# Kernel tuning notes

Measured on AMD Instinct MI355X. Metric: run time of the kernel, lower is better.

## Reference

```python
import jax, jax.numpy as jnp
import numpy as np

N_NODES, N_EDGES = 10000, 100000
NODE_DIM, NUM_BASIS = 128, 20
MULS = {0: 128, 1: 64, 2: 32}            # 128x0e + 64x1e + 32x2e
NUM_IRREPS = 224                          # total multiplicity count
HIDDEN = NODE_DIM + NUM_IRREPS            # 352
SPH_DIM = 128 * 1 + 64 * 3 + 32 * 5       # 480
LN_EPS = 1e-5

def _s2_basis():
    # orthonormal (Frobenius) basis of symmetric traceless 3x3 matrices (real l=2)
    s = np.zeros((5, 3, 3)); r2 = 1.0 / np.sqrt(2.0)
    s[0, 0, 1] = s[0, 1, 0] = r2
    s[1, 1, 2] = s[1, 2, 1] = r2
    s[2] = np.diag([-1.0, -1.0, 2.0]) / np.sqrt(6.0)
    s[3, 0, 2] = s[3, 2, 0] = r2
    s[4] = np.diag([1.0, -1.0, 0.0]) * r2
    return s

def _cg_tables():
    # real Clebsch-Gordan tensors for l<=2 built from the invariant tensors
    # delta, Levi-Civita, and the symmetric-traceless basis; unit Frobenius norm (e3nn w3j convention)
    e3 = np.zeros((3, 3, 3))
    e3[0, 1, 2] = e3[1, 2, 0] = e3[2, 0, 1] = 1.0
    e3[0, 2, 1] = e3[2, 1, 0] = e3[1, 0, 2] = -1.0
    S = _s2_basis(); I3 = np.eye(3); I5 = np.eye(5)
    nrm = lambda c: (c / np.linalg.norm(c)).astype(np.float32)
    cg = {(0, 0, 0): np.ones((1, 1, 1), np.float32)}
    cg[(0, 1, 1)] = nrm(I3[None]); cg[(1, 0, 1)] = nrm(I3[:, None, :]); cg[(1, 1, 0)] = nrm(I3[:, :, None])
    cg[(0, 2, 2)] = nrm(I5[None]); cg[(2, 0, 2)] = nrm(I5[:, None, :]); cg[(2, 2, 0)] = nrm(I5[:, :, None])
    cg[(1, 1, 1)] = nrm(e3)
    cg[(1, 1, 2)] = nrm(np.transpose(S, (1, 2, 0)))
    cg[(1, 2, 1)] = nrm(np.transpose(S, (1, 0, 2)))
    cg[(2, 1, 1)] = nrm(S)
    cg[(2, 2, 1)] = nrm(np.einsum('ijk,Mil,Nlj->MNk', e3, S, S))
    cg[(1, 2, 2)] = nrm(np.einsum('iab,Mac,Ncb->iMN', e3, S, S))
    cg[(2, 1, 2)] = nrm(np.einsum('jab,Mac,Ncb->MjN', e3, S, S))
    cg[(2, 2, 2)] = nrm(np.einsum('Mab,Nbc,Pca->MNP', S, S, S))
    return cg

CG = _cg_tables()
PATHS = [(0, 0, 0), (1, 1, 0), (2, 2, 0),
         (0, 1, 1), (1, 0, 1), (1, 1, 1), (1, 2, 1), (2, 1, 1), (2, 2, 1),
         (0, 2, 2), (1, 1, 2), (1, 2, 2), (2, 0, 2), (2, 1, 2), (2, 2, 2)]
FAN = {0: 224, 1: 384, 2: 352}   # e3nn 'element' path-norm fan-in per output irrep
TP_NUMW = sum(MULS[l1] * MULS[l3] for (l1, _, l3) in PATHS)

def _layernorm(x, w, b):
    mu = x.mean(-1, keepdims=True)
    var = ((x - mu) ** 2).mean(-1, keepdims=True)
    return (x - mu) * jax.lax.rsqrt(var + LN_EPS) * w + b

def _o3_layernorm(x, w, b):
    # equivariant layer norm: per-irrep RMS over (mul, m); mean-centering + bias only for scalars
    n = x.shape[0]; outs = []; off = 0; woff = 0
    for l in (0, 1, 2):
        mul, d = MULS[l], 2 * l + 1
        f = x[:, off:off + mul * d].reshape(n, mul, d)
        if l == 0:
            f = f - f.mean(axis=1, keepdims=True)
        nrm = (f * f).mean(axis=(1, 2), keepdims=True)
        f = f * jax.lax.rsqrt(nrm + LN_EPS) * w[woff:woff + mul][None, :, None]
        if l == 0:
            f = f + b[None, :, None]
        outs.append(f.reshape(n, mul * d)); off += mul * d; woff += mul
    return jnp.concatenate(outs, -1)

def _fc_tp(x1, x2, tp_w):
    # FullyConnectedTensorProduct(128x0e+64x1e+32x2e, 1x0e+1x1e+1x2e -> 128x0e+64x1e+32x2e)
    outs = {0: 0.0, 1: 0.0, 2: 0.0}; off = 0
    for (l1, l2, l3) in PATHS:
        m1, m3 = MULS[l1], MULS[l3]
        W = tp_w[off:off + m1 * m3].reshape(m1, m3); off += m1 * m3
        pw = float(np.sqrt((2 * l3 + 1) / FAN[l3]))
        outs[l3] = outs[l3] + pw * jnp.einsum('eum,en,mnk,uw->ewk', x1[l1], x2[l2], jnp.asarray(CG[(l1, l2, l3)]), W, optimize=True)
    e = x2[0].shape[0]
    return jnp.concatenate([outs[l].reshape(e, -1) for l in (0, 1, 2)], -1)

def _forward(x_scalar, x_spherical, rbf, rsh, ln_w, ln_b, o3_w, o3_b,
             mlp_w1, mlp_b1, mlp_w2, mlp_b2, rbf_w, tp_w, edge_index):
    scalar_in = _layernorm(x_scalar, ln_w, ln_b)                # [N,128]
    spherical_in = _o3_layernorm(x_spherical, o3_w, o3_b)       # [N,480]
    h = jax.nn.silu(scalar_in @ mlp_w1 + mlp_b1)
    scalar_out = h @ mlp_w2 + mlp_b2                            # [N,352]
    filt = rbf @ rbf_w                                          # [E,352]
    dst, src = edge_index[0], edge_index[1]
    fo = scalar_out[src] * filt                                 # gather + RBF filter
    gate, msg_scalar = fo[:, :NUM_IRREPS], fo[:, NUM_IRREPS:]
    sph = spherical_in[src]                                     # [E,480]
    e = sph.shape[0]
    # ElementwiseTensorProduct(edge_irreps, 224x0e): per-channel scalar gating
    x1 = {0: (sph[:, :128] * gate[:, :128])[:, :, None],
          1: sph[:, 128:320].reshape(e, 64, 3) * gate[:, 128:192, None],
          2: sph[:, 320:480].reshape(e, 32, 5) * gate[:, 192:224, None]}
    x2 = {0: rsh[:, :1], 1: rsh[:, 1:4], 2: rsh[:, 4:9]}
    msg_sph = _fc_tp(x1, x2, tp_w)                              # [E,480]
    new_scalar = scalar_in.at[dst].add(msg_scalar)
    new_spherical = spherical_in.at[dst].add(msg_sph)
    return new_scalar, new_spherical

def setup_inputs():
    key = jax.random.key(0)
    ks = jax.random.split(key, 9)
    return {
        'x_scalar': jax.random.normal(ks[0], (N_NODES, NODE_DIM), jnp.float32),
        'x_spherical': jax.random.normal(ks[1], (N_NODES, SPH_DIM), jnp.float32),
        'rbf': jax.random.uniform(ks[2], (N_EDGES, NUM_BASIS), jnp.float32),
        'rsh': jax.random.normal(ks[3], (N_EDGES, 9), jnp.float32),
        'edge_index': jax.random.randint(ks[4], (2, N_EDGES), 0, N_NODES, dtype=jnp.int32),
        'ln_w': jnp.ones((NODE_DIM,), jnp.float32),
        'ln_b': jnp.zeros((NODE_DIM,), jnp.float32),
        'o3_w': jnp.ones((NUM_IRREPS,), jnp.float32),
        'o3_b': jnp.zeros((128,), jnp.float32),
        'mlp_w1': jax.random.normal(ks[5], (NODE_DIM, NODE_DIM), jnp.float32) / np.sqrt(NODE_DIM),
        'mlp_b1': jnp.zeros((NODE_DIM,), jnp.float32),
        'mlp_w2': jax.random.normal(ks[6], (NODE_DIM, HIDDEN), jnp.float32) / np.sqrt(NODE_DIM),
        'mlp_b2': jnp.zeros((HIDDEN,), jnp.float32),
        'rbf_w': jax.random.normal(ks[7], (NUM_BASIS, HIDDEN), jnp.float32) / np.sqrt(NUM_BASIS),
        'tp_w': jax.random.normal(ks[8], (TP_NUMW,), jnp.float32),
    }

def reference(x_scalar, x_spherical, rbf, rsh, edge_index, ln_w, ln_b, o3_w, o3_b,
              mlp_w1, mlp_b1, mlp_w2, mlp_b2, rbf_w, tp_w):
    return _forward(x_scalar, x_spherical, rbf, rsh, ln_w, ln_b, o3_w, o3_b,
                    mlp_w1, mlp_b1, mlp_w2, mlp_b2, rbf_w, tp_w, edge_index)
```

## Files before the change

### kernel.cpp

```cpp
#include <hip/hip_runtime.h>

#define NN 10000
#define NE 100000
#define ND 128
#define NB 20
#define NIR 224
#define NH 352
#define SD 480
#define BS 512
#define ET 16
#define NTILES (NE / ET)

#define CR   0.70710678118654752f
#define CA   0.40824829046386302f
#define HA   0.20412414523193151f
#define HR   0.35355339059327376f
#define C110 0.57735026918962576f
#define C220 0.44721359549995794f
#define C111 0.40824829046386302f
#define C11X 0.44721359549995794f
#define C221 0.36514837167011074f
#define C222 0.58554004376912270f
#define S32  0.86602540378443865f
#define PW0  0.066815310478106094f
#define PW1  0.088388347648318447f
#define PW2  0.11918321088232916f

typedef __bf16 v8bf __attribute__((ext_vector_type(8)));
typedef unsigned short us8v __attribute__((ext_vector_type(8)));
typedef float f32x4 __attribute__((ext_vector_type(4)));

__device__ __forceinline__ unsigned short f2bfc(float f) {
  __bf16 h = (__bf16)f;
  return __builtin_bit_cast(unsigned short, h);
}
__device__ __forceinline__ float bf2f(unsigned short h) {
  unsigned int u = ((unsigned int)h) << 16;
  return __builtin_bit_cast(float, u);
}

__device__ __forceinline__ float warpReduceSum(float v) {
  #pragma unroll
  for (int off = 32; off > 0; off >>= 1) v += __shfl_down(v, off, 64);
  return v;
}

__device__ __forceinline__ int t2tT(int t) {
  if (t < 128) return t;
  if (t < 320) { int c = t - 128; return 128 + (c % 3) * 64 + c / 3; }
  int c = t - 320; return 320 + (c % 5) * 32 + c / 5;
}

__global__ __launch_bounds__(256) void sort_hist(const int* __restrict__ ei, int* __restrict__ cnt) {
  int e = blockIdx.x * 256 + threadIdx.x;
  if (e < NE) atomicAdd(&cnt[ei[e]], 1);
}

__global__ __launch_bounds__(1024) void sort_scan(const int* __restrict__ cnt, int* __restrict__ cursor) {
  __shared__ int part[1024];
  const int t = threadIdx.x;
  int loc[10]; int s = 0;
  #pragma unroll
  for (int j = 0; j < 10; ++j) { int idx = t * 10 + j; int v = (idx < NN) ? cnt[idx] : 0; loc[j] = s; s += v; }
  part[t] = s; __syncthreads();
  for (int d = 1; d < 1024; d <<= 1) {
    int v = (t >= d) ? part[t - d] : 0; __syncthreads();
    part[t] += v; __syncthreads();
  }
  int off = part[t] - s;
  #pragma unroll
  for (int j = 0; j < 10; ++j) { int idx = t * 10 + j; if (idx < NN) cursor[idx] = off + loc[j]; }
}

__global__ __launch_bounds__(256) void sort_scatter(
    const int* __restrict__ ei, int* __restrict__ cursor, int* __restrict__ es_eid) {
  int e = blockIdx.x * 256 + threadIdx.x;
  if (e < NE) {
    int d = ei[e];
    int pos = atomicAdd(&cursor[d], 1);
    es_eid[pos] = e;
  }
}

__global__ __launch_bounds__(128) void node_ln_kernel(
    const float* __restrict__ xs, const float* __restrict__ xsph,
    const float* __restrict__ lnw, const float* __restrict__ lnb,
    const float* __restrict__ o3w, const float* __restrict__ o3b,
    float* __restrict__ s_in, float* __restrict__ sphT,
    float* __restrict__ out0)
{
  const int n = blockIdx.x, t = threadIdx.x;
  __shared__ float red[4];

  auto reduce2 = [&](float a, float b) {
// ... 43 lines not shown
    const float* __restrict__ b2, float* __restrict__ s_out)
{
  __shared__ float sIn[NPB][ND];
  __shared__ float sH[NPB][ND];
  const int t = threadIdx.x;
  const int n0 = blockIdx.x * NPB;
  for (int i = t; i < NPB * ND; i += 256) sIn[i >> 7][i & 127] = s_in[n0 * ND + i];
  __syncthreads();
  {
    const int j = t & 127, g = t >> 7;
    float acc[4] = {0.f, 0.f, 0.f, 0.f};
    for (int k = 0; k < ND; ++k) {
      float w = w1[k * ND + j];
      #pragma unroll
      for (int i = 0; i < 4; ++i) acc[i] = fmaf(sIn[g + 2 * i][k], w, acc[i]);
    }
    #pragma unroll
    for (int i = 0; i < 4; ++i) {
      float z = acc[i] + b1[j];
      sH[g + 2 * i][j] = z / (1.f + __expf(-z));
    }
  }
  __syncthreads();
  for (int jb = 0; jb < 2; ++jb) {
    int j = jb * 256 + t;
    if (j < NH) {
      float acc[NPB];
      #pragma unroll
      for (int i = 0; i < NPB; ++i) acc[i] = b2[j];
      for (int k = 0; k < ND; ++k) {
        float w = w2[k * NH + j];
        #pragma unroll
        for (int i = 0; i < NPB; ++i) acc[i] = fmaf(sH[i][k], w, acc[i]);
      }
      #pragma unroll
      for (int i = 0; i < NPB; ++i) s_out[(n0 + i) * NH + j] = acc[i];
    }
  }
}

__device__ __forceinline__ float wc0(const float* w, int u, int j) {
  int off = (u < 128) ? u * 128 : (u < 192) ? 16384 + (u - 128) * 128 : 24576 + (u - 192) * 128;
  return w[off + j];
}
__device__ __forceinline__ float wc1(const float* w, int u, int j) {
  int off = (u < 128) ? 28672 + u * 64 : (u < 192) ? 36864 + (u - 128) * 64
          : (u < 256) ? 40960 + (u - 192) * 64 : (u < 320) ? 45056 + (u - 256) * 64
          : (u < 352) ? 49152 + (u - 320) * 64 : 51200 + (u - 352) * 64;
  return w[off + j];
}
__device__ __forceinline__ float wc2(const float* w, int u, int j) {
  int off = (u < 128) ? 53248 + u * 32 : (u < 192) ? 57344 + (u - 128) * 32
          : (u < 256) ? 59392 + (u - 192) * 32 : (u < 288) ? 61440 + (u - 256) * 32
          : (u < 320) ? 62464 + (u - 288) * 32 : 63488 + (u - 320) * 32;
  return w[off + j];
}

__global__ __launch_bounds__(256) void prep_w_kernel(
    const float* __restrict__ tpw, const float* __restrict__ rbf_w,
    unsigned short* __restrict__ W0g, unsigned short* __restrict__ W1g,
    unsigned short* __restrict__ W2g, unsigned short* __restrict__ Wfq)
{
  int gid = blockIdx.x * 256 + threadIdx.x;
  int i = gid & 7, lane = (gid >> 3) & 63;
  int r = lane & 15, kl = lane >> 4;
  if (gid < 28672) {
    int fid = gid >> 9, kk = fid >> 3, wid = fid & 7;
    W0g[gid] = f2bfc(wc0(tpw, kk * 32 + kl * 8 + i, wid * 16 + r));
  } else if (gid < 53248) {
    int g = gid - 28672, fid = g >> 9, kk = fid >> 2, nt = fid & 3;
    W1g[g] = f2bfc(wc1(tpw, kk * 32 + kl * 8 + i, nt * 16 + r));
  } else if (gid < 65536) {
    int g = gid - 53248, fid = g >> 9, q = fid >> 2, kh = (fid >> 1) & 1, ntc = fid & 1;
    int kk = kh * 6 + q;
    W2g[g] = (kk < 11) ? f2bfc(wc2(tpw, kk * 32 + kl * 8 + i, ntc * 16 + r)) : (unsigned short)0;
  } else if (gid < 77824) {
    int g = gid - 65536, fid = g >> 9, q = fid >> 3, wid = fid & 7;
    int t22 = wid + q * 8, k = kl * 8 + i;
    Wfq[g] = (t22 < 22 && k < 20) ? f2bfc(rbf_w[k * NH + t22 * 16 + r]) : (unsigned short)0;
  }
}

template<int M>
__device__ __forceinline__ void emit_dot(unsigned short* dst, const unsigned short* x1,
                                         const int* offs, const float* cf) {
  us8v xv[M];
  #pragma unroll
  for (int m = 0; m < M; ++m) xv[m] = *(const us8v*)&x1[offs[m]];
  v8bf o;
  #pragma unroll
  for (int i = 0; i < 8; ++i) {
    float a = 0.f;
    #pragma unroll
    for (int m = 0; m < M; ++m) a = fmaf(cf[m], bf2f(xv[m][i]), a);
    o[i] = (__bf16)a;
  }
  *(us8v*)dst = __builtin_bit_cast(us8v, o);
}

#define TSW(e, idx) ((idx) ^ (((e) & 7) << 3))

__device__ __forceinline__ void build0_item(unsigned short* Tb, const unsigned short* x1,
                                            const float* R, int e, int ub) {
  int u0 = ub * 8;
  unsigned short* dst = Tb + TSW(e, e * 384 + u0);
  if (u0 < 128) {
    float cf[1] = { PW0 * R[0] };
    int offs[1] = { u0 };
    emit_dot<1>(dst, x1, offs, cf);
  } else if (u0 < 192) {
    int m0 = u0 - 128;
    float cf[3] = { PW0 * C110 * R[1], PW0 * C110 * R[2], PW0 * C110 * R[3] };
    int offs[3] = { 128 + m0, 192 + m0, 256 + m0 };
    emit_dot<3>(dst, x1, offs, cf);
  } else {
    int m0 = u0 - 192;
    float cf[5] = { PW0 * C220 * R[4], PW0 * C220 * R[5], PW0 * C220 * R[6],
                    PW0 * C220 * R[7], PW0 * C220 * R[8] };
    int offs[5] = { 320 + m0, 352 + m0, 384 + m0, 416 + m0, 448 + m0 };
    emit_dot<5>(dst, x1, offs, cf);
  }
}

template<int k>
__device__ __forceinline__ void build1_item(unsigned short* Tb, const unsigned short* x1,
                                            const float* R, int e, int ub) {
  int u0 = ub * 8;
  unsigned short* dst = Tb + TSW(e, e * 384 + u0);
  const float s = R[0], v0 = R[1], v1 = R[2], v2 = R[3];
  const float w0 = R[4], w1 = R[5], w2 = R[6], w3 = R[7], w4 = R[8];
  if (u0 < 128) {
    float cf[1] = { PW1 * C110 * R[1 + k] };
    int offs[1] = { u0 };
    emit_dot<1>(dst, x1, offs, cf);
  } else if (u0 < 192) {
    float cf[1] = { PW1 * C110 * s };
    int offs[1] = { 128 + k * 64 + (u0 - 128) };
    emit_dot<1>(dst, x1, offs, cf);
  } else if (u0 < 256) {
    constexpr int ka = (k + 1) % 3, kb = (k + 2) % 3;
    int m0 = u0 - 192;
    float cf[2] = { PW1 * C111 * R[1 + kb], -PW1 * C111 * R[1 + ka] };
    int offs[2] = { 128 + ka * 64 + m0, 128 + kb * 64 + m0 };
    emit_dot<2>(dst, x1, offs, cf);
  } else if (u0 < 320) {
    int m0 = u0 - 256;
    float cf[3];
    if constexpr (k == 0) { cf[0] = PW1*C11X*(-CA*w2 + CR*w4); cf[1] = PW1*C11X*CR*w0; cf[2] = PW1*C11X*CR*w3; }
    else if constexpr (k == 1) { cf[0] = PW1*C11X*CR*w0; cf[1] = PW1*C11X*(-CA*w2 - CR*w4); cf[2] = PW1*C11X*CR*w1; }
    else { cf[0] = PW1*C11X*CR*w3; cf[1] = PW1*C11X*CR*w1; cf[2] = PW1*C11X*2.f*CA*w2; }
    int offs[3] = { 128 + m0, 192 + m0, 256 + m0 };
    emit_dot<3>(dst, x1, offs, cf);
  } else if (u0 < 352) {
    int m0 = u0 - 320;
    if constexpr (k == 0) {
      float cf[4] = { PW1*C11X*CR*v1, PW1*C11X*(-CA*v0), PW1*C11X*CR*v2, PW1*C11X*CR*v0 };
      int offs[4] = { 320 + m0, 384 + m0, 416 + m0, 448 + m0 };
      emit_dot<4>(dst, x1, offs, cf);
    } else if constexpr (k == 1) {
      float cf[4] = { PW1*C11X*CR*v0, PW1*C11X*CR*v2, PW1*C11X*(-CA*v1), PW1*C11X*(-CR*v1) };
      int offs[4] = { 320 + m0, 352 + m0, 384 + m0, 448 + m0 };
      emit_dot<4>(dst, x1, offs, cf);
    } else {
      float cf[3] = { PW1*C11X*CR*v1, PW1*C11X*2.f*CA*v2, PW1*C11X*CR*v0 };
      int offs[3] = { 352 + m0, 384 + m0, 416 + m0 };
      emit_dot<3>(dst, x1, offs, cf);
    }
  } else {
    int m0 = u0 - 352;
    if constexpr (k == 0) {
      float cf[5] = { PW1*C221*0.5f*w3, PW1*C221*(S32*w2 + 0.5f*w4), PW1*C221*(-S32*w1),
                      PW1*C221*(-0.5f*w0), PW1*C221*(-0.5f*w1) };
      int offs[5] = { 320 + m0, 352 + m0, 384 + m0, 416 + m0, 448 + m0 };
      emit_dot<5>(dst, x1, offs, cf);
    } else if constexpr (k == 1) {
      float cf[5] = { PW1*C221*(-0.5f*w1), PW1*C221*0.5f*w0, PW1*C221*S32*w3,
                      PW1*C221*(-S32*w2 + 0.5f*w4), PW1*C221*(-0.5f*w3) };
      int offs[5] = { 320 + m0, 352 + m0, 384 + m0, 416 + m0, 448 + m0 };
      emit_dot<5>(dst, x1, offs, cf);
    } else {
      float cf[4] = { PW1*C221*(-w4), PW1*C221*(-0.5f*w3), PW1*C221*0.5f*w1, PW1*C221*w0 };
      int offs[4] = { 320 + m0, 352 + m0, 416 + m0, 448 + m0 };
      emit_dot<4>(dst, x1, offs, cf);
    }
  }
}

template<int K>
__device__ __forceinline__ void build2_item(unsigned short* Tb, const unsigned short* x1,
                                            const float* R, int e, int ub) {
  int u0 = ub * 8;
  unsigned short* dst = Tb + TSW(e, e * 384 + u0);
  const float s = R[0], v0 = R[1], v1 = R[2], v2 = R[3];
  const float w0 = R[4], w1 = R[5], w2 = R[6], w3 = R[7], w4 = R[8];
  if (u0 < 128) {
    float cf[1] = { PW2 * C220 * R[4 + K] };
    int offs[1] = { u0 };
    emit_dot<1>(dst, x1, offs, cf);
  } else if (u0 < 192) {
    int m0 = u0 - 128;
    if constexpr (K == 0) {
      float cf[2] = { PW2*C11X*CR*v1, PW2*C11X*CR*v0 };
      int offs[2] = { 128 + m0, 192 + m0 };
      emit_dot<2>(dst, x1, offs, cf);
    } else if constexpr (K == 1) {
      float cf[2] = { PW2*C11X*CR*v2, PW2*C11X*CR*v1 };
      int offs[2] = { 192 + m0, 256 + m0 };
      emit_dot<2>(dst, x1, offs, cf);
    } else if constexpr (K == 2) {
      float cf[3] = { PW2*C11X*(-CA*v0), PW2*C11X*(-CA*v1), PW2*C11X*2.f*CA*v2 };
      int offs[3] = { 128 + m0, 192 + m0, 256 + m0 };
      emit_dot<3>(dst, x1, offs, cf);
    } else if constexpr (K == 3) {
      float cf[2] = { PW2*C11X*CR*v2, PW2*C11X*CR*v0 };
      int offs[2] = { 128 + m0, 256 + m0 };
      emit_dot<2>(dst, x1, offs, cf);
    } else {
      float cf[2] = { PW2*C11X*CR*v0, PW2*C11X*(-CR*v1) };
      int offs[2] = { 128 + m0, 192 + m0 };
      emit_dot<2>(dst, x1, offs, cf);
    }
  } else if (u0 < 256) {
    int m0 = u0 - 192;
    if constexpr (K == 2) {
      float cf[2] = { PW2*C221*S32*w1, PW2*C221*(-S32*w3) };
      int offs[2] = { 128 + m0, 192 + m0 };
      emit_dot<2>(dst, x1, offs, cf);
    } else {
      float cf[3];
      if constexpr (K == 0) { cf[0]=PW2*C221*(-0.5f*w3); cf[1]=PW2*C221*0.5f*w1; cf[2]=PW2*C221*w4; }
      else if constexpr (K == 1) { cf[0]=PW2*C221*(-S32*w2 - 0.5f*w4); cf[1]=PW2*C221*(-0.5f*w0); cf[2]=PW2*C221*0.5f*w3; }
      else if constexpr (K == 3) { cf[0]=PW2*C221*0.5f*w0; cf[1]=PW2*C221*(S32*w2 - 0.5f*w4); cf[2]=PW2*C221*(-0.5f*w1); }
      else { cf[0]=PW2*C221*0.5f*w1; cf[1]=PW2*C221*0.5f*w3; cf[2]=PW2*C221*(-w0); }
      int offs[3] = { 128 + m0, 192 + m0, 256 + m0 };
      emit_dot<3>(dst, x1, offs, cf);
    }
  } else if (u0 < 288) {
    int m0 = u0 - 256;
    float cf[1] = { PW2 * C220 * s };
    int offs[1] = { 320 + K * 32 + m0 };
    emit_dot<1>(dst, x1, offs, cf);
  } else if (u0 < 320) {
    int m0 = u0 - 288;
    if constexpr (K == 0) {
      float cf[3] = { PW2*C221*0.5f*v1, PW2*C221*(-0.5f*v0), PW2*C221*v2 };
      int offs[3] = { 352 + m0, 416 + m0, 448 + m0 };
      emit_dot<3>(dst, x1, offs, cf);
    } else if constexpr (K == 1) {
      float cf[4] = { PW2*C221*(-0.5f*v1), PW2*C221*(-S32*v0), PW2*C221*0.5f*v2, PW2*C221*(-0.5f*v0) };
      int offs[4] = { 320 + m0, 384 + m0, 416 + m0, 448 + m0 };
      emit_dot<4>(dst, x1, offs, cf);
    } else if constexpr (K == 2) {
      float cf[2] = { PW2*C221*S32*v0, PW2*C221*(-S32*v1) };
      int offs[2] = { 352 + m0, 416 + m0 };
      emit_dot<2>(dst, x1, offs, cf);
    } else if constexpr (K == 3) {
      float cf[4] = { PW2*C221*0.5f*v0, PW2*C221*(-0.5f*v2), PW2*C221*S32*v1, PW2*C221*(-0.5f*v1) };
      int offs[4] = { 320 + m0, 352 + m0, 384 + m0, 448 + m0 };
      emit_dot<4>(dst, x1, offs, cf);
    } else {
      float cf[3] = { PW2*C221*(-v2), PW2*C221*0.5f*v0, PW2*C221*0.5f*v1 };
      int offs[3] = { 320 + m0, 352 + m0, 416 + m0 };
      emit_dot<3>(dst, x1, offs, cf);
    }
  } else {
    int m0 = u0 - 320;
    if constexpr (K == 0) {
      float cf[4] = { PW2*C222*(-CA*w2), PW2*C222*HR*w3, PW2*C222*(-CA*w0), PW2*C222*HR*w1 };
      int offs[4] = { 320 + m0, 352 + m0, 384 + m0, 416 + m0 };
      emit_dot<4>(dst, x1, offs, cf);
    } else if constexpr (K == 4) {
      float cf[4] = { PW2*C222*(-HR*w1), PW2*C222*(-CA*w4), PW2*C222*HR*w3, PW2*C222*(-CA*w2) };
      int offs[4] = { 352 + m0, 384 + m0, 416 + m0, 448 + m0 };
      emit_dot<4>(dst, x1, offs, cf);
    } else {
      float cf[5];
      if constexpr (K == 1) { cf[0]=PW2*C222*HR*w3; cf[1]=PW2*C222*(HA*w2 - HR*w4); cf[2]=PW2*C222*HA*w1; cf[3]=PW2*C222*HR*w0; cf[4]=PW2*C222*(-HR*w1); }
      else if constexpr (K == 2) { cf[0]=PW2*C222*(-CA*w0); cf[1]=PW2*C222*HA*w1; cf[2]=PW2*C222*CA*w2; cf[3]=PW2*C222*HA*w3; cf[4]=PW2*C222*(-CA*w4); }
      else { cf[0]=PW2*C222*HR*w1; cf[1]=PW2*C222*HR*w0; cf[2]=PW2*C222*HA*w3; cf[3]=PW2*C222*(HA*w2 + HR*w4); cf[4]=PW2*C222*HR*w3; }
      int offs[5] = { 320 + m0, 352 + m0, 384 + m0, 416 + m0, 448 + m0 };
      emit_dot<5>(dst, x1, offs, cf);
    }
  }
}

__global__ __launch_bounds__(BS, 4) void tp_fused_kernel(
    const float* __restrict__ rbf, const float* __restrict__ rsh,
    const int* __restrict__ ei, const float* __restrict__ s_out,
    const float* __restrict__ sphT,
    const unsigned short* __restrict__ W0g, const unsigned short* __restrict__ W1g,
    const unsigned short* __restrict__ W2g, const unsigned short* __restrict__ Wfq,
    float* __restrict__ out0, unsigned short* __restrict__ msgT)
{
  __shared__ __align__(16) unsigned char smem[65216];
  unsigned short* S0 = (unsigned short*)smem;
  unsigned short* S1 = (unsigned short*)(smem + 12288);
  unsigned short* S2 = (unsigned short*)(smem + 24576);
  unsigned short* S3 = (unsigned short*)(smem + 36864);
  unsigned short* gateU = (unsigned short*)smem;
  unsigned short* rbfpadU = (unsigned short*)(smem + 12288);
  unsigned short* X1u = (unsigned short*)(smem + 49152);
  float* RshF = (float*)(smem + 64512);
  int* EdstS = (int*)(smem + 65088);
  int* EsrcS = (int*)(smem + 65152);

  const int tid = threadIdx.x;
  const int wid = tid >> 6, lane = tid & 63;
  const int r = lane & 15, kl = lane >> 4;
  const int be = tid >> 5, th = tid & 31;

  auto MFMA = [](v8bf a, v8bf b, f32x4 c) {
    return __builtin_amdgcn_mfma_f32_16x16x32_bf16(a, b, c, 0, 0, 0);
  };
  auto ldw = [&](const unsigned short* base, int fid) {
    return __builtin_bit_cast(v8bf, *(const us8v*)&base[fid * 512 + lane * 8]);
  };

  auto mfma_l0 = [&](const unsigned short* T, long ebase) {
    f32x4 acc = {0.f, 0.f, 0.f, 0.f};
    #pragma unroll
    for (int kk = 0; kk < 7; ++kk) {
      v8bf b = ldw(W0g, kk * 8 + wid);
      us8v a = *(const us8v*)&T[TSW(r, r * 384 + kl * 8 + kk * 32)];
      acc = MFMA(__builtin_bit_cast(v8bf, a), b, acc);
    }
    int col = wid * 16 + r;
    #pragma unroll
    for (int j = 0; j < 4; ++j)
      msgT[(ebase + kl * 4 + j) * SD + col] = f2bfc(acc[j]);
  };

  auto mfma_l1w = [&](const unsigned short* T, int k, int nt, long ebase) {
    f32x4 acc = {0.f, 0.f, 0.f, 0.f};
    #pragma unroll
    for (int kk = 0; kk < 12; ++kk) {
      v8bf b = ldw(W1g, kk * 4 + nt);
      us8v a = *(const us8v*)&T[TSW(r, r * 384 + kl * 8 + kk * 32)];
      acc = MFMA(__builtin_bit_cast(v8bf, a), b, acc);
    }
    int col = 128 + k * 64 + nt * 16 + r;
    #pragma unroll
    for (int j = 0; j < 4; ++j)
      msgT[(ebase + kl * 4 + j) * SD + col] = f2bfc(acc[j]);
  };

  auto mfma_l2w = [&](const unsigned short* T, int K, int ntc, long ebase) {
    f32x4 acc = {0.f, 0.f, 0.f, 0.f};
    #pragma unroll
    for (int kk = 0; kk < 11; ++kk) {
      v8bf b = ldw(W2g, (kk % 6) * 4 + (kk / 6) * 2 + ntc);
      us8v a = *(const us8v*)&T[TSW(r, r * 384 + kk * 32 + kl * 8)];
      acc = MFMA(__builtin_bit_cast(v8bf, a), b, acc);
    }
    int col = 320 + K * 32 + ntc * 16 + r;
    #pragma unroll
    for (int j = 0; j < 4; ++j)
      msgT[(ebase + kl * 4 + j) * SD + col] = f2bfc(acc[j]);
  };

  for (int tile = blockIdx.x; tile < NTILES; tile += gridDim.x) {
    const int e0 = tile * ET;
    const long ebase = e0;
    for (int i = tid; i < ET; i += BS) { EdstS[i] = ei[e0 + i]; EsrcS[i] = ei[NE + e0 + i]; }
    for (int i = tid; i < ET * 9; i += BS) RshF[i] = rsh[(long)e0 * 9 + i];
    for (int i = tid; i < ET * 32; i += BS) {
      int e = i >> 5, b = i & 31;
      rbfpadU[e * 40 + b] = (b < 20) ? f2bfc(rbf[(long)(e0 + e) * NB + b]) : (unsigned short)0;
    }
    __syncthreads();
    {
      us8v ra = *(const us8v*)&rbfpadU[r * 40 + kl * 8];
      v8bf av = __builtin_bit_cast(v8bf, ra);
      #pragma unroll
      for (int q = 0; q < 3; ++q) {
        int t22 = wid + q * 8;
        if (t22 < 22) {
          v8bf b = ldw(Wfq, q * 8 + wid);
          f32x4 acc = {0.f, 0.f, 0.f, 0.f};
          acc = MFMA(av, b, acc);
          int gi = t22 * 16 + r;
          #pragma unroll
          for (int j = 0; j < 4; ++j) {
            int e = kl * 4 + j;
            float so = s_out[(long)EsrcS[e] * NH + gi];
            float val = acc[j] * so;
            if (t22 < 14) gateU[e * 232 + gi] = f2bfc(val);
            else unsafeAtomicAdd(&out0[(long)EdstS[e] * ND + (gi - 224)], val);
          }
        }
      }
    }
    __syncthreads();
    float Rr[9];
    #pragma unroll
    for (int j = 0; j < 9; ++j) Rr[j] = RshF[be * 9 + j];
    const unsigned short* x1p = &X1u[be * 480];
    {
      long srow = (long)EsrcS[be] * SD;
      #pragma unroll
      for (int rep = 0; rep < 2; ++rep) {
        int cb = th + rep * 32;
        if (rep == 0 || th < 28) {
          int c0 = cb * 8;
          int gidx = (c0 < 128) ? c0 : (c0 < 320) ? 128 + (c0 & 63) : 192 + (c0 & 31);
          us8v gv = *(const us8v*)&gateU[be * 232 + gidx];
          const float4 sa = *(const float4*)&sphT[srow + c0];
          const float4 sb = *(const float4*)&sphT[srow + c0 + 4];
          float sv[8] = {sa.x, sa.y, sa.z, sa.w, sb.x, sb.y, sb.z, sb.w};
          v8bf o;
          #pragma unroll
          for (int i = 0; i < 8; ++i) o[i] = (__bf16)(sv[i] * bf2f(gv[i]));
          *(us8v*)&X1u[be * 480 + c0] = __builtin_bit_cast(us8v, o);
        }
      }
    }
    __syncthreads();
    if (th < 28) build0_item(S0, x1p, Rr, be, th);
    __syncthreads();
    build1_item<0>(S1, x1p, Rr, be, th);
    if (th < 16) build1_item<0>(S1, x1p, Rr, be, th + 32);
    else         build1_item<1>(S2, x1p, Rr, be, th - 16);
    build1_item<1>(S2, x1p, Rr, be, th + 16);
    mfma_l0(S0, ebase);
    __syncthreads();
    build1_item<2>(S3, x1p, Rr, be, th);
    if (th < 16) build1_item<2>(S3, x1p, Rr, be, th + 32);
    else         build2_item<0>(S0, x1p, Rr, be, th - 16);
    if (th < 28) build2_item<0>(S0, x1p, Rr, be, th + 16);
    if (wid < 4) mfma_l1w(S1, 0, wid, ebase);
    else         mfma_l1w(S2, 1, wid - 4, ebase);
    __syncthreads();
    build2_item<1>(S1, x1p, Rr, be, th);
    if (th < 12) build2_item<1>(S1, x1p, Rr, be, th + 32);
    else         build2_item<2>(S2, x1p, Rr, be, th - 12);
    if (th < 24) build2_item<2>(S2, x1p, Rr, be, th + 20);
    if (wid < 4)      mfma_l1w(S3, 2, wid, ebase);
    else if (wid < 6) mfma_l2w(S0, 0, wid - 4, ebase);
    __syncthreads();
    build2_item<3>(S3, x1p, Rr, be, th);
    if (th < 12) build2_item<3>(S3, x1p, Rr, be, th + 32);
    else         build2_item<4>(S0, x1p, Rr, be, th - 12);
    if (th < 24) build2_item<4>(S0, x1p, Rr, be, th + 20);
    if (wid < 2)      mfma_l2w(S1, 1, wid, ebase);
    else if (wid < 4) mfma_l2w(S2, 2, wid - 2, ebase);
    __syncthreads();
    if (wid < 2)      mfma_l2w(S3, 3, wid, ebase);
    else if (wid < 4) mfma_l2w(S0, 4, wid - 2, ebase);
    __syncthreads();
  }
}

__global__ __launch_bounds__(512) void gather_kernel(
    const float* __restrict__ sphT, const unsigned short* __restrict__ msgT,
    const int* __restrict__ cnt, const int* __restrict__ cursor,
    const int* __restrict__ es_eid, float* __restrict__ out1)
{
  __shared__ float sumT[SD];
  __shared__ int eids[160];
  __shared__ int s_deg;
  const int n = blockIdx.x, t = threadIdx.x;
  if (t == 0) {
    int d = cnt[n];
    s_deg = (d > 160) ? 160 : d;
  }
  __syncthreads();
  int deg = s_deg;
  int start = cursor[n] - cnt[n];
  for (int i = t; i < deg; i += 512) eids[i] = es_eid[start + i];
  __syncthreads();
  if (t < 240) {
    float a0 = 0.f, a1 = 0.f;
    for (int i = 0; i < deg; ++i) {
      unsigned v = *(const unsigned*)&msgT[(long)eids[i] * SD + 2 * t];
      a0 += bf2f((unsigned short)(v & 0xffffu));
      a1 += bf2f((unsigned short)(v >> 16));
    }
    sumT[2 * t] = a0; sumT[2 * t + 1] = a1;
  }
  __syncthreads();
  if (t < SD) {
    int tT = t2tT(t);
    out1[(long)n * SD + t] = sphT[(long)n * SD + tT] + sumT[tT];
  }
}

extern "C" void kernel_launch(void* const* d_in, const int* in_sizes, int n_in,
                              void* d_out, int out_size, void* d_ws, size_t ws_size,
                              hipStream_t stream)
{
  const float* xs   = (const float*)d_in[0];
  const float* xsph = (const float*)d_in[1];
  const float* rbf  = (const float*)d_in[2];
  const float* rsh  = (const float*)d_in[3];
  const int*   ei   = (const int*)d_in[4];
  const float* lnw  = (const float*)d_in[5];
  const float* lnb  = (const float*)d_in[6];
  const float* o3w  = (const float*)d_in[7];
  const float* o3b  = (const float*)d_in[8];
  const float* w1   = (const float*)d_in[9];
  const float* b1   = (const float*)d_in[10];
  const float* w2   = (const float*)d_in[11];
  const float* b2   = (const float*)d_in[12];
  const float* rbfw = (const float*)d_in[13];
  const float* tpw  = (const float*)d_in[14];

  float* out0 = (float*)d_out;
  float* out1 = out0 + (size_t)NN * ND;

  float* ws      = (float*)d_ws;
  float* s_in    = ws;
  float* sphT    = ws + (size_t)NN * ND;
  float* s_out   = ws + (size_t)NN * (ND + SD);
  unsigned short* msgT = (unsigned short*)(ws + (size_t)NN * (ND + SD + NH));
  unsigned short* wbase = msgT + (size_t)NE * SD;
  unsigned short* W0g = wbase;
  unsigned short* W1g = wbase + 28672;
  unsigned short* W2g = wbase + 53248;
  unsigned short* Wfq = wbase + 65536;
  int* ibase  = (int*)(wbase + 77824);
  int* cnt    = ibase;
  int* cursor = ibase + 10000;
  int* es_eid = ibase + 20000;

  hipMemsetAsync(cnt, 0, (size_t)NN * sizeof(int), stream);
  sort_hist<<<(NE + 255) / 256, 256, 0, stream>>>(ei, cnt);
  sort_scan<<<1, 1024, 0, stream>>>(cnt, cursor);
  sort_scatter<<<(NE + 255) / 256, 256, 0, stream>>>(ei, cursor, es_eid);
  prep_w_kernel<<<304, 256, 0, stream>>>(tpw, rbfw, W0g, W1g, W2g, Wfq);
  node_ln_kernel<<<NN, 128, 0, stream>>>(xs, xsph, lnw, lnb, o3w, o3b, s_in, sphT, out0);
  mlp_kernel<<<NN / NPB, 256, 0, stream>>>(s_in, w1, b1, w2, b2, s_out);
  tp_fused_kernel<<<512, BS, 0, stream>>>(rbf, rsh, ei, s_out, sphT,
                                          W0g, W1g, W2g, Wfq, out0, msgT);
  gather_kernel<<<NN, 512, 0, stream>>>(sphT, msgT, cnt, cursor, es_eid, out1);
}
```

Measured before the change: 660.6 us.

## Build MFMA A-fragments in registers instead of staging through LDS

```diff
diff --git a/kernel.cpp b/kernel.cpp
--- a/kernel.cpp
+++ b/kernel.cpp
@@ -10,6 +10,7 @@
 #define BS 512
 #define ET 16
 #define NTILES (NE / ET)
+#define XSTR 488
 
 #define CR   0.70710678118654752f
 #define CA   0.40824829046386302f
@@ -219,8 +220,7 @@
 }
 
 template<int M>
-__device__ __forceinline__ void emit_dot(unsigned short* dst, const unsigned short* x1,
-                                         const int* offs, const float* cf) {
+__device__ __forceinline__ v8bf dot_frag(const unsigned short* x1, const int* offs, const float* cf) {
   us8v xv[M];
   #pragma unroll
   for (int m = 0; m < M; ++m) xv[m] = *(const us8v*)&x1[offs[m]];
@@ -232,137 +232,127 @@
     for (int m = 0; m < M; ++m) a = fmaf(cf[m], bf2f(xv[m][i]), a);
     o[i] = (__bf16)a;
   }
-  *(us8v*)dst = __builtin_bit_cast(us8v, o);
-}
-
-#define TSW(e, idx) ((idx) ^ (((e) & 7) << 3))
-
-__device__ __forceinline__ void build0_item(unsigned short* Tb, const unsigned short* x1,
-                                            const float* R, int e, int ub) {
-  int u0 = ub * 8;
-  unsigned short* dst = Tb + TSW(e, e * 384 + u0);
-  if (u0 < 128) {
+  return o;
+}
+
+template<int BASE>
+__device__ __forceinline__ v8bf b0frag(const unsigned short* x1, const float* R, int kl8) {
+  if constexpr (BASE < 128) {
     float cf[1] = { PW0 * R[0] };
-    int offs[1] = { u0 };
-    emit_dot<1>(dst, x1, offs, cf);
-  } else if (u0 < 192) {
-    int m0 = u0 - 128;
+    int offs[1] = { BASE + kl8 };
+    return dot_frag<1>(x1, offs, cf);
+  } else if constexpr (BASE < 192) {
+    int m0 = BASE - 128 + kl8;
     float cf[3] = { PW0 * C110 * R[1], PW0 * C110 * R[2], PW0 * C110 * R[3] };
     int offs[3] = { 128 + m0, 192 + m0, 256 + m0 };
-    emit_dot<3>(dst, x1, offs, cf);
+    return dot_frag<3>(x1, offs, cf);
   } else {
-    int m0 = u0 - 192;
+    int m0 = BASE - 192 + kl8;
     float cf[5] = { PW0 * C220 * R[4], PW0 * C220 * R[5], PW0 * C220 * R[6],
                     PW0 * C220 * R[7], PW0 * C220 * R[8] };
     int offs[5] = { 320 + m0, 352 + m0, 384 + m0, 416 + m0, 448 + m0 };
-    emit_dot<5>(dst, x1, offs, cf);
-  }
-}
-
-template<int k>
-__device__ __forceinline__ void build1_item(unsigned short* Tb, const unsigned short* x1,
-                                            const float* R, int e, int ub) {
-  int u0 = ub * 8;
-  unsigned short* dst = Tb + TSW(e, e * 384 + u0);
+    return dot_frag<5>(x1, offs, cf);
+  }
+}
+
+template<int k, int BASE>
+__device__ __forceinline__ v8bf b1frag(const unsigned short* x1, const float* R, int kl8) {
   const float s = R[0], v0 = R[1], v1 = R[2], v2 = R[3];
   const float w0 = R[4], w1 = R[5], w2 = R[6], w3 = R[7], w4 = R[8];
-  if (u0 < 128) {
+  if constexpr (BASE < 128) {
     float cf[1] = { PW1 * C110 * R[1 + k] };
-    int offs[1] = { u0 };
-    emit_dot<1>(dst, x1, offs, cf);
-  } else if (u0 < 192) {
+    int offs[1] = { BASE + kl8 };
+    return dot_frag<1>(x1, offs, cf);
+  } else if constexpr (BASE < 192) {
     float cf[1] = { PW1 * C110 * s };
-    int offs[1] = { 128 + k * 64 + (u0 - 128) };
-    emit_dot<1>(dst, x1, offs, cf);
-  } else if (u0 < 256) {
+    int offs[1] = { 128 + k * 64 + (BASE - 128) + kl8 };
+    return dot_frag<1>(x1, offs, cf);
+  } else if constexpr (BASE < 256) {
     constexpr int ka = (k + 1) % 3, kb = (k + 2) % 3;
-    int m0 = u0 - 192;
+    int m0 = BASE - 192 + kl8;
     float cf[2] = { PW1 * C111 * R[1 + kb], -PW1 * C111 * R[1 + ka] };
     int offs[2] = { 128 + ka * 64 + m0, 128 + kb * 64 + m0 };
-    emit_dot<2>(dst, x1, offs, cf);
-  } else if (u0 < 320) {
-    int m0 = u0 - 256;
+    return dot_frag<2>(x1, offs, cf);
+  } else if constexpr (BASE < 320) {
+    int m0 = BASE - 256 + kl8;
     float cf[3];
     if constexpr (k == 0) { cf[0] = PW1*C11X*(-CA*w2 + CR*w4); cf[1] = PW1*C11X*CR*w0; cf[2] = PW1*C11X*CR*w3; }
     else if constexpr (k == 1) { cf[0] = PW1*C11X*CR*w0; cf[1] = PW1*C11X*(-CA*w2 - CR*w4); cf[2] = PW1*C11X*CR*w1; }
     else { cf[0] = PW1*C11X*CR*w3; cf[1] = PW1*C11X*CR*w1; cf[2] = PW1*C11X*2.f*CA*w2; }
     int offs[3] = { 128 + m0, 192 + m0, 256 + m0 };
-    emit_dot<3>(dst, x1, offs, cf);
-  } else if (u0 < 352) {
-    int m0 = u0 - 320;
+    return dot_frag<3>(x1, offs, cf);
+  } else if constexpr (BASE < 352) {
+    int m0 = BASE - 320 + kl8;
     if constexpr (k == 0) {
       float cf[4] = { PW1*C11X*CR*v1, PW1*C11X*(-CA*v0), PW1*C11X*CR*v2, PW1*C11X*CR*v0 };
       int offs[4] = { 320 + m0, 384 + m0, 416 + m0, 448 + m0 };
-      emit_dot<4>(dst, x1, offs, cf);
+      return dot_frag<4>(x1, offs, cf);
     } else if constexpr (k == 1) {
       float cf[4] = { PW1*C11X*CR*v0, PW1*C11X*CR*v2, PW1*C11X*(-CA*v1), PW1*C11X*(-CR*v1) };
       int offs[4] = { 320 + m0, 352 + m0, 384 + m0, 448 + m0 };
-      emit_dot<4>(dst, x1, offs, cf);
+      return dot_frag<4>(x1, offs, cf);
     } else {
       float cf[3] = { PW1*C11X*CR*v1, PW1*C11X*2.f*CA*v2, PW1*C11X*CR*v0 };
       int offs[3] = { 352 + m0, 384 + m0, 416 + m0 };
-      emit_dot<3>(dst, x1, offs, cf);
+      return dot_frag<3>(x1, offs, cf);
     }
   } else {
-    int m0 = u0 - 352;
+    int m0 = BASE - 352 + kl8;
     if constexpr (k == 0) {
       float cf[5] = { PW1*C221*0.5f*w3, PW1*C221*(S32*w2 + 0.5f*w4), PW1*C221*(-S32*w1),
                       PW1*C221*(-0.5f*w0), PW1*C221*(-0.5f*w1) };
       int offs[5] = { 320 + m0, 352 + m0, 384 + m0, 416 + m0, 448 + m0 };
-      emit_dot<5>(dst, x1, offs, cf);
+      return dot_frag<5>(x1, offs, cf);
     } else if constexpr (k == 1) {
       float cf[5] = { PW1*C221*(-0.5f*w1), PW1*C221*0.5f*w0, PW1*C221*S32*w3,
                       PW1*C221*(-S32*w2 + 0.5f*w4), PW1*C221*(-0.5f*w3) };
       int offs[5] = { 320 + m0, 352 + m0, 384 + m0, 416 + m0, 448 + m0 };
-      emit_dot<5>(dst, x1, offs, cf);
+      return dot_frag<5>(x1, offs, cf);
     } else {
       float cf[4] = { PW1*C221*(-w4), PW1*C221*(-0.5f*w3), PW1*C221*0.5f*w1, PW1*C221*w0 };
       int offs[4] = { 320 + m0, 352 + m0, 416 + m0, 448 + m0 };
-      emit_dot<4>(dst, x1, offs, cf);
-    }
-  }
-}
-
-template<int K>
-__device__ __forceinline__ void build2_item(unsigned short* Tb, const unsigned short* x1,
-                                            const float* R, int e, int ub) {
-  int u0 = ub * 8;
-  unsigned short* dst = Tb + TSW(e, e * 384 + u0);
+      return dot_frag<4>(x1, offs, cf);
+    }
+  }
+}
+
+template<int K, int BASE>
+__device__ __forceinline__ v8bf b2frag(const unsigned short* x1, const float* R, int kl8) {
   const float s = R[0], v0 = R[1], v1 = R[2], v2 = R[3];
   const float w0 = R[4], w1 = R[5], w2 = R[6], w3 = R[7], w4 = R[8];
-  if (u0 < 128) {
+  if constexpr (BASE < 128) {
     float cf[1] = { PW2 * C220 * R[4 + K] };
-    int offs[1] = { u0 };
-    emit_dot<1>(dst, x1, offs, cf);
-  } else if (u0 < 192) {
-    int m0 = u0 - 128;
+    int offs[1] = { BASE + kl8 };
+    return dot_frag<1>(x1, offs, cf);
+  } else if constexpr (BASE < 192) {
+    int m0 = BASE - 128 + kl8;
     if constexpr (K == 0) {
       float cf[2] = { PW2*C11X*CR*v1, PW2*C11X*CR*v0 };
       int offs[2] = { 128 + m0, 192 + m0 };
-      emit_dot<2>(dst, x1, offs, cf);
+      return dot_frag<2>(x1, offs, cf);
     } else if constexpr (K == 1) {
       float cf[2] = { PW2*C11X*CR*v2, PW2*C11X*CR*v1 };
       int offs[2] = { 192 + m0, 256 + m0 };
-      emit_dot<2>(dst, x1, offs, cf);
+      return dot_frag<2>(x1, offs, cf);
     } else if constexpr (K == 2) {
       float cf[3] = { PW2*C11X*(-CA*v0), PW2*C11X*(-CA*v1), PW2*C11X*2.f*CA*v2 };
       int offs[3] = { 128 + m0, 192 + m0, 256 + m0 };
-      emit_dot<3>(dst, x1, offs, cf);
+      return dot_frag<3>(x1, offs, cf);
     } else if constexpr (K == 3) {
       float cf[2] = { PW2*C11X*CR*v2, PW2*C11X*CR*v0 };
       int offs[2] = { 128 + m0, 256 + m0 };
-      emit_dot<2>(dst, x1, offs, cf);
+      return dot_frag<2>(x1, offs, cf);
     } else {
       float cf[2] = { PW2*C11X*CR*v0, PW2*C11X*(-CR*v1) };
       int offs[2] = { 128 + m0, 192 + m0 };
-      emit_dot<2>(dst, x1, offs, cf);
-    }
-  } else if (u0 < 256) {
-    int m0 = u0 - 192;
+      return dot_frag<2>(x1, offs, cf);
+    }
+  } else if constexpr (BASE < 256) {
+    int m0 = BASE - 192 + kl8;
     if constexpr (K == 2) {
       float cf[2] = { PW2*C221*S32*w1, PW2*C221*(-S32*w3) };
       int offs[2] = { 128 + m0, 192 + m0 };
-      emit_dot<2>(dst, x1, offs, cf);
+      return dot_frag<2>(x1, offs, cf);
     } else {
       float cf[3];
       if constexpr (K == 0) { cf[0]=PW2*C221*(-0.5f*w3); cf[1]=PW2*C221*0.5f*w1; cf[2]=PW2*C221*w4; }
@@ -370,55 +360,104 @@
       else if constexpr (K == 3) { cf[0]=PW2*C221*0.5f*w0; cf[1]=PW2*C221*(S32*w2 - 0.5f*w4); cf[2]=PW2*C221*(-0.5f*w1); }
       else { cf[0]=PW2*C221*0.5f*w1; cf[1]=PW2*C221*0.5f*w3; cf[2]=PW2*C221*(-w0); }
       int offs[3] = { 128 + m0, 192 + m0, 256 + m0 };
-      emit_dot<3>(dst, x1, offs, cf);
-    }
-  } else if (u0 < 288) {
-    int m0 = u0 - 256;
+      return dot_frag<3>(x1, offs, cf);
+    }
+  } else if constexpr (BASE < 288) {
+    int m0 = BASE - 256 + kl8;
     float cf[1] = { PW2 * C220 * s };
     int offs[1] = { 320 + K * 32 + m0 };
-    emit_dot<1>(dst, x1, offs, cf);
-  } else if (u0 < 320) {
-    int m0 = u0 - 288;
+    return dot_frag<1>(x1, offs, cf);
+  } else if constexpr (BASE < 320) {
+    int m0 = BASE - 288 + kl8;
     if constexpr (K == 0) {
       float cf[3] = { PW2*C221*0.5f*v1, PW2*C221*(-0.5f*v0), PW2*C221*v2 };
       int offs[3] = { 352 + m0, 416 + m0, 448 + m0 };
-      emit_dot<3>(dst, x1, offs, cf);
+      return dot_frag<3>(x1, offs, cf);
     } else if constexpr (K == 1) {
       float cf[4] = { PW2*C221*(-0.5f*v1), PW2*C221*(-S32*v0), PW2*C221*0.5f*v2, PW2*C221*(-0.5f*v0) };
       int offs[4] = { 320 + m0, 384 + m0, 416 + m0, 448 + m0 };
-      emit_dot<4>(dst, x1, offs, cf);
+      return dot_frag<4>(x1, offs, cf);
     } else if constexpr (K == 2) {
       float cf[2] = { PW2*C221*S32*v0, PW2*C221*(-S32*v1) };
       int offs[2] = { 352 + m0, 416 + m0 };
-      emit_dot<2>(dst, x1, offs, cf);
+      return dot_frag<2>(x1, offs, cf);
     } else if constexpr (K == 3) {
       float cf[4] = { PW2*C221*0.5f*v0, PW2*C221*(-0.5f*v2), PW2*C221*S32*v1, PW2*C221*(-0.5f*v1) };
       int offs[4] = { 320 + m0, 352 + m0, 384 + m0, 448 + m0 };
-      emit_dot<4>(dst, x1, offs, cf);
+      return dot_frag<4>(x1, offs, cf);
     } else {
       float cf[3] = { PW2*C221*(-v2), PW2*C221*0.5f*v0, PW2*C221*0.5f*v1 };
       int offs[3] = { 320 + m0, 352 + m0, 416 + m0 };
-      emit_dot<3>(dst, x1, offs, cf);
+      return dot_frag<3>(x1, offs, cf);
     }
   } else {
-    int m0 = u0 - 320;
+    int m0 = BASE - 320 + kl8;
     if constexpr (K == 0) {
       float cf[4] = { PW2*C222*(-CA*w2), PW2*C222*HR*w3, PW2*C222*(-CA*w0), PW2*C222*HR*w1 };
       int offs[4] = { 320 + m0, 352 + m0, 384 + m0, 416 + m0 };
-      emit_dot<4>(dst, x1, offs, cf);
+      return dot_frag<4>(x1, offs, cf);
     } else if constexpr (K == 4) {
       float cf[4] = { PW2*C222*(-HR*w1), PW2*C222*(-CA*w4), PW2*C222*HR*w3, PW2*C222*(-CA*w2) };
       int offs[4] = { 352 + m0, 384 + m0, 416 + m0, 448 + m0 };
-      emit_dot<4>(dst, x1, offs, cf);
+      return dot_frag<4>(x1, offs, cf);
     } else {
       float cf[5];
       if constexpr (K == 1) { cf[0]=PW2*C222*HR*w3; cf[1]=PW2*C222*(HA*w2 - HR*w4); cf[2]=PW2*C222*HA*w1; cf[3]=PW2*C222*HR*w0; cf[4]=PW2*C222*(-HR*w1); }
       else if constexpr (K == 2) { cf[0]=PW2*C222*(-CA*w0); cf[1]=PW2*C222*HA*w1; cf[2]=PW2*C222*CA*w2; cf[3]=PW2*C222*HA*w3; cf[4]=PW2*C222*(-CA*w4); }
       else { cf[0]=PW2*C222*HR*w1; cf[1]=PW2*C222*HR*w0; cf[2]=PW2*C222*HA*w3; cf[3]=PW2*C222*(HA*w2 + HR*w4); cf[4]=PW2*C222*HR*w3; }
       int offs[5] = { 320 + m0, 352 + m0, 384 + m0, 416 + m0, 448 + m0 };
-      emit_dot<5>(dst, x1, offs, cf);
-    }
-  }
+      return dot_frag<5>(x1, offs, cf);
+    }
+  }
+}
+
+__device__ __forceinline__ f32x4 MFMAf(v8bf a, v8bf b, f32x4 c) {
+  return __builtin_amdgcn_mfma_f32_16x16x32_bf16(a, b, c, 0, 0, 0);
+}
+__device__ __forceinline__ v8bf ldwf(const unsigned short* base, int fid, int lane) {
+  return __builtin_bit_cast(v8bf, *(const us8v*)&base[fid * 512 + lane * 8]);
+}
+
+__device__ __forceinline__ void job_l0(const unsigned short* x1, const float* R, int kl8,
+    int nt, int r, int kl, int lane, long ebase,
+    const unsigned short* __restrict__ W0g, unsigned short* __restrict__ msgT) {
+  f32x4 acc = {0.f, 0.f, 0.f, 0.f};
+  #define L0S(KK) acc = MFMAf(b0frag<KK * 32>(x1, R, kl8), ldwf(W0g, KK * 8 + nt, lane), acc);
+  L0S(0) L0S(1) L0S(2) L0S(3) L0S(4) L0S(5) L0S(6)
+  #undef L0S
+  int col = nt * 16 + r;
+  #pragma unroll
+  for (int j = 0; j < 4; ++j)
+    msgT[(ebase + kl * 4 + j) * SD + col] = f2bfc(acc[j]);
+}
+
+template<int k>
+__device__ __forceinline__ void job_l1(const unsigned short* x1, const float* R, int kl8,
+    int nt, int r, int kl, int lane, long ebase,
+    const unsigned short* __restrict__ W1g, unsigned short* __restrict__ msgT) {
+  f32x4 acc = {0.f, 0.f, 0.f, 0.f};
+  #define L1S(KK) acc = MFMAf(b1frag<k, KK * 32>(x1, R, kl8), ldwf(W1g, KK * 4 + nt, lane), acc);
+  L1S(0) L1S(1) L1S(2) L1S(3) L1S(4) L1S(5) L1S(6) L1S(7) L1S(8) L1S(9) L1S(10) L1S(11)
+  #undef L1S
+  int col = 128 + k * 64 + nt * 16 + r;
+  #pragma unroll
+  for (int j = 0; j < 4; ++j)
+    msgT[(ebase + kl * 4 + j) * SD + col] = f2bfc(acc[j]);
+}
+
+template<int K>
+__device__ __forceinline__ void job_l2(const unsigned short* x1, const float* R, int kl8,
+    int ntc, int r, int kl, int lane, long ebase,
+    const unsigned short* __restrict__ W2g, unsigned short* __restrict__ msgT) {
+  f32x4 acc = {0.f, 0.f, 0.f, 0.f};
+  #define L2S(KK) acc = MFMAf(b2frag<K, KK * 32>(x1, R, kl8), \
+                              ldwf(W2g, (KK % 6) * 4 + (KK / 6) * 2 + ntc, lane), acc);
+  L2S(0) L2S(1) L2S(2) L2S(3) L2S(4) L2S(5) L2S(6) L2S(7) L2S(8) L2S(9) L2S(10)
+  #undef L2S
+  int col = 320 + K * 32 + ntc * 16 + r;
+  #pragma unroll
+  for (int j = 0; j < 4; ++j)
+    msgT[(ebase + kl * 4 + j) * SD + col] = f2bfc(acc[j]);
 }
 
 __global__ __launch_bounds__(BS, 4) void tp_fused_kernel(
@@ -429,71 +468,18 @@
     const unsigned short* __restrict__ W2g, const unsigned short* __restrict__ Wfq,
     float* __restrict__ out0, unsigned short* __restrict__ msgT)
 {
-  __shared__ __align__(16) unsigned char smem[65216];
-  unsigned short* S0 = (unsigned short*)smem;
-  unsigned short* S1 = (unsigned short*)(smem + 12288);
-  unsigned short* S2 = (unsigned short*)(smem + 24576);
-  unsigned short* S3 = (unsigned short*)(smem + 36864);
+  __shared__ __align__(16) unsigned char smem[25024];
   unsigned short* gateU = (unsigned short*)smem;
-  unsigned short* rbfpadU = (unsigned short*)(smem + 12288);
-  unsigned short* X1u = (unsigned short*)(smem + 49152);
-  float* RshF = (float*)(smem + 64512);
-  int* EdstS = (int*)(smem + 65088);
-  int* EsrcS = (int*)(smem + 65152);
+  unsigned short* rbfpadU = (unsigned short*)(smem + 7424);
+  unsigned short* X1u = (unsigned short*)(smem + 8704);
+  float* RshF = (float*)(smem + 24320);
+  int* EdstS = (int*)(smem + 24896);
+  int* EsrcS = (int*)(smem + 24960);
 
   const int tid = threadIdx.x;
   const int wid = tid >> 6, lane = tid & 63;
-  const int r = lane & 15, kl = lane >> 4;
+  const int r = lane & 15, kl = lane >> 4, kl8 = kl * 8;
   const int be = tid >> 5, th = tid & 31;
-
-  auto MFMA = [](v8bf a, v8bf b, f32x4 c) {
-    return __builtin_amdgcn_mfma_f32_16x16x32_bf16(a, b, c, 0, 0, 0);
-  };
-  auto ldw = [&](const unsigned short* base, int fid) {
-    return __builtin_bit_cast(v8bf, *(const us8v*)&base[fid * 512 + lane * 8]);
-  };
-
-  auto mfma_l0 = [&](const unsigned short* T, long ebase) {
-    f32x4 acc = {0.f, 0.f, 0.f, 0.f};
-    #pragma unroll
-    for (int kk = 0; kk < 7; ++kk) {
-      v8bf b = ldw(W0g, kk * 8 + wid);
-      us8v a = *(const us8v*)&T[TSW(r, r * 384 + kl * 8 + kk * 32)];
-      acc = MFMA(__builtin_bit_cast(v8bf, a), b, acc);
-    }
-    int col = wid * 16 + r;
-    #pragma unroll
-    for (int j = 0; j < 4; ++j)
-      msgT[(ebase + kl * 4 + j) * SD + col] = f2bfc(acc[j]);
-  };
-
-  auto mfma_l1w = [&](const unsigned short* T, int k, int nt, long ebase) {
-    f32x4 acc = {0.f, 0.f, 0.f, 0.f};
-    #pragma unroll
-    for (int kk = 0; kk < 12; ++kk) {
-      v8bf b = ldw(W1g, kk * 4 + nt);
-      us8v a = *(const us8v*)&T[TSW(r, r * 384 + kl * 8 + kk * 32)];
-      acc = MFMA(__builtin_bit_cast(v8bf, a), b, acc);
-    }
-    int col = 128 + k * 64 + nt * 16 + r;
-    #pragma unroll
-    for (int j = 0; j < 4; ++j)
-      msgT[(ebase + kl * 4 + j) * SD + col] = f2bfc(acc[j]);
-  };
-
-  auto mfma_l2w = [&](const unsigned short* T, int K, int ntc, long ebase) {
-    f32x4 acc = {0.f, 0.f, 0.f, 0.f};
-    #pragma unroll
-    for (int kk = 0; kk < 11; ++kk) {
-      v8bf b = ldw(W2g, (kk % 6) * 4 + (kk / 6) * 2 + ntc);
-      us8v a = *(const us8v*)&T[TSW(r, r * 384 + kk * 32 + kl * 8)];
-      acc = MFMA(__builtin_bit_cast(v8bf, a), b, acc);
-    }
-    int col = 320 + K * 32 + ntc * 16 + r;
-    #pragma unroll
-    for (int j = 0; j < 4; ++j)
-      msgT[(ebase + kl * 4 + j) * SD + col] = f2bfc(acc[j]);
-  };
 
   for (int tile = blockIdx.x; tile < NTILES; tile += gridDim.x) {
     const int e0 = tile * ET;
@@ -506,15 +492,15 @@
     }
     __syncthreads();
     {
-      us8v ra = *(const us8v*)&rbfpadU[r * 40 + kl * 8];
+      us8v ra = *(const us8v*)&rbfpadU[r * 40 + kl8];
       v8bf av = __builtin_bit_cast(v8bf, ra);
       #pragma unroll
       for (int q = 0; q < 3; ++q) {
         int t22 = wid + q * 8;
         if (t22 < 22) {
-          v8bf b = ldw(Wfq, q * 8 + wid);
+          v8bf b = ldwf(Wfq, q * 8 + wid, lane);
           f32x4 acc = {0.f, 0.f, 0.f, 0.f};
-          acc = MFMA(av, b, acc);
+          acc = MFMAf(av, b, acc);
           int gi = t22 * 16 + r;
           #pragma unroll
           for (int j = 0; j < 4; ++j) {
@@ -528,10 +514,6 @@
       }
     }
     __syncthreads();
-    float Rr[9];
-    #pragma unroll
-    for (int j = 0; j < 9; ++j) Rr[j] = RshF[be * 9 + j];
-    const unsigned short* x1p = &X1u[be * 480];
     {
       long srow = (long)EsrcS[be] * SD;
       #pragma unroll
@@ -547,42 +529,35 @@
           v8bf o;
           #pragma unroll
           for (int i = 0; i < 8; ++i) o[i] = (__bf16)(sv[i] * bf2f(gv[i]));
-          *(us8v*)&X1u[be * 480 + c0] = __builtin_bit_cast(us8v, o);
+          *(us8v*)&X1u[be * XSTR + c0] = __builtin_bit_cast(us8v, o);
         }
       }
     }
     __syncthreads();
-    if (th < 28) build0_item(S0, x1p, Rr, be, th);
-    __syncthreads();
-    build1_item<0>(S1, x1p, Rr, be, th);
-    if (th < 16) build1_item<0>(S1, x1p, Rr, be, th + 32);
-    else         build1_item<1>(S2, x1p, Rr, be, th - 16);
-    build1_item<1>(S2, x1p, Rr, be, th + 16);
-    mfma_l0(S0, ebase);
-    __syncthreads();
-    build1_item<2>(S3, x1p, Rr, be, th);
-    if (th < 16) build1_item<2>(S3, x1p, Rr, be, th + 32);
-    else         build2_item<0>(S0, x1p, Rr, be, th - 16);
-    if (th < 28) build2_item<0>(S0, x1p, Rr, be, th + 16);
-    if (wid < 4) mfma_l1w(S1, 0, wid, ebase);
-    else         mfma_l1w(S2, 1, wid - 4, ebase);
-    __syncthreads();
-    build2_item<1>(S1, x1p, Rr, be, th);
-    if (th < 12) build2_item<1>(S1, x1p, Rr, be, th + 32);
-    else         build2_item<2>(S2, x1p, Rr, be, th - 12);
-    if (th < 24) build2_item<2>(S2, x1p, Rr, be, th + 20);
-    if (wid < 4)      mfma_l1w(S3, 2, wid, ebase);
-    else if (wid < 6) mfma_l2w(S0, 0, wid - 4, ebase);
-    __syncthreads();
-    build2_item<3>(S3, x1p, Rr, be, th);
-    if (th < 12) build2_item<3>(S3, x1p, Rr, be, th + 32);
-    else         build2_item<4>(S0, x1p, Rr, be, th - 12);
-    if (th < 24) build2_item<4>(S0, x1p, Rr, be, th + 20);
-    if (wid < 2)      mfma_l2w(S1, 1, wid, ebase);
-    else if (wid < 4) mfma_l2w(S2, 2, wid - 2, ebase);
-    __syncthreads();
-    if (wid < 2)      mfma_l2w(S3, 3, wid, ebase);
-    else if (wid < 4) mfma_l2w(S0, 4, wid - 2, ebase);
+    {
+      float Rl[9];
+      #pragma unroll
+      for (int j = 0; j < 9; ++j) Rl[j] = RshF[r * 9 + j];
+      const unsigned short* x1r = &X1u[r * XSTR];
+
+      job_l0(x1r, Rl, kl8, wid, r, kl, lane, ebase, W0g, msgT);
+      if (wid < 4) {
+        job_l1<0>(x1r, Rl, kl8, wid, r, kl, lane, ebase, W1g, msgT);
+        job_l1<2>(x1r, Rl, kl8, wid, r, kl, lane, ebase, W1g, msgT);
+      } else {
+        job_l1<1>(x1r, Rl, kl8, wid - 4, r, kl, lane, ebase, W1g, msgT);
+      }
+      if (wid == 0)      job_l2<4>(x1r, Rl, kl8, 0, r, kl, lane, ebase, W2g, msgT);
+      else if (wid == 1) job_l2<4>(x1r, Rl, kl8, 1, r, kl, lane, ebase, W2g, msgT);
+      else if (wid == 4) { job_l2<0>(x1r, Rl, kl8, 0, r, kl, lane, ebase, W2g, msgT);
+                           job_l2<2>(x1r, Rl, kl8, 0, r, kl, lane, ebase, W2g, msgT); }
+      else if (wid == 5) { job_l2<0>(x1r, Rl, kl8, 1, r, kl, lane, ebase, W2g, msgT);
+                           job_l2<2>(x1r, Rl, kl8, 1, r, kl, lane, ebase, W2g, msgT); }
+      else if (wid == 6) { job_l2<1>(x1r, Rl, kl8, 0, r, kl, lane, ebase, W2g, msgT);
+                           job_l2<3>(x1r, Rl, kl8, 0, r, kl, lane, ebase, W2g, msgT); }
+      else if (wid == 7) { job_l2<1>(x1r, Rl, kl8, 1, r, kl, lane, ebase, W2g, msgT);
+                           job_l2<3>(x1r, Rl, kl8, 1, r, kl, lane, ebase, W2g, msgT); }
+    }
     __syncthreads();
   }
 }
@@ -666,7 +641,7 @@
   prep_w_kernel<<<304, 256, 0, stream>>>(tpw, rbfw, W0g, W1g, W2g, Wfq);
   node_ln_kernel<<<NN, 128, 0, stream>>>(xs, xsph, lnw, lnb, o3w, o3b, s_in, sphT, out0);
   mlp_kernel<<<NN / NPB, 256, 0, stream>>>(s_in, w1, b1, w2, b2, s_out);
-  tp_fused_kernel<<<512, BS, 0, stream>>>(rbf, rsh, ei, s_out, sphT,
-                                          W0g, W1g, W2g, Wfq, out0, msgT);
+  tp_fused_kernel<<<1024, BS, 0, stream>>>(rbf, rsh, ei, s_out, sphT,
+                                           W0g, W1g, W2g, Wfq, out0, msgT);
   gather_kernel<<<NN, 512, 0, stream>>>(sphT, msgT, cnt, cursor, es_eid, out1);
 }
```

New measurement: 1.226 ms. +85.5%, slower.
